# Optimization experiments

Hardware: AMD Instinct MI355X
Metric: run time of the kernel (lower is better)

Reference implementation:

```python
import jax, jax.numpy as jnp
import numpy as np

CUTOFF = 3.0   # self.cutoff
RMIN = 3.5     # rmin in cutoff_function (note rmin > cutoff, faithful to source)
ETA = 4.0
N_RADIAL = 5
N_3BODY = 12
NATOMS = 2048
K = 48         # neighbors per atom (equal counts -> ragged loop becomes dense batch)
HID = 64
NPAIRS = NATOMS * K


def setup_inputs() -> dict:
    key = jax.random.key(0)
    ks = jax.random.split(key, 4)
    # displacements scaled so |rij| is mostly within a few Angstrom
    rij = jax.random.normal(ks[0], (NPAIRS, 3), jnp.float32) * 1.5
    # sorted-by-atom pair list with K neighbors per atom
    unique_i = jnp.repeat(jnp.arange(NATOMS, dtype=jnp.int64), K)
    W1 = jax.random.normal(ks[1], (N_RADIAL + N_3BODY, HID), jnp.float32) * 0.1
    b1 = jnp.zeros((HID,), jnp.float32)
    W2 = jax.random.normal(ks[2], (HID, HID), jnp.float32) * 0.1
    b2 = jnp.zeros((HID,), jnp.float32)
    W3 = jax.random.normal(ks[3], (HID, 1), jnp.float32) * 0.1
    b3 = jnp.zeros((1,), jnp.float32)
    return dict(rij=rij, unique_i=unique_i, W1=W1, b1=b1, W2=W2, b2=b2, W3=W3, b3=b3)


def _energy(rij, W1, b1, W2, b2, W3, b3):
    d = jnp.linalg.norm(rij, axis=1, keepdims=True)           # (P,1)
    diff_norm = rij / jnp.maximum(d, 1e-12)                   # F.normalize
    # pair cutoff (rmin=3.5, c=3.0 as in source)
    fc = jnp.where(d > RMIN,
                   0.5 + 0.5 * jnp.cos(jnp.pi * (d - RMIN) / (CUTOFF - RMIN)),
                   1.0)
    # radial Bessel basis, n = 1..5
    ns = jnp.arange(1, N_RADIAL + 1, dtype=rij.dtype)
    rbf = jnp.sqrt(2.0 / CUTOFF) * jnp.sin(ns * jnp.pi / CUTOFF * d) / d * fc  # (P,5)
    # 3-body Gaussian descriptors
    fcrik = (0.5 + 0.5 * jnp.cos(jnp.pi * d / CUTOFF))[:, 0]  # (P,)
    dn = diff_norm.reshape(NATOMS, K, 3)
    cosang = jnp.einsum('nkd,nld->nkl', dn, dn)               # (N,K,K) pairwise mm
    cosang = jnp.where(jnp.eye(K, dtype=bool)[None], 0.0, cosang)  # fill_diagonal_(0)
    mu = jnp.linspace(-1.0, 1.0, N_3BODY).astype(rij.dtype)
    w = fcrik.reshape(NATOMS, 1, K, 1)                        # fcrik broadcast on axis being summed
    g3b = jnp.sum(jnp.exp(-ETA * (cosang[..., None] - mu) ** 2) * w, axis=2)  # (N,K,12)
    g3b = g3b.reshape(NPAIRS, N_3BODY)
    desc = jnp.concatenate([rbf, g3b], axis=1)                # (P,17)
    h = jnp.tanh(desc @ W1 + b1)
    h = jnp.tanh(h @ W2 + b2)
    eij = h @ W3 + b3                                         # (P,1)
    return jnp.sum(eij * fc)


def reference(rij, unique_i, W1, b1, W2, b2, W3, b3):
    # Module output: gradients of total energy w.r.t. rij (written into beta)
    return jax.grad(_energy)(rij, W1, b1, W2, b2, W3, b3)
```

## Files before the change

### kernel.cpp

```cpp
#include <hip/hip_runtime.h>
#include <hip/hip_bf16.h>

#define NATOMS 2048
#define K 48
#define P (NATOMS * K)
#define NR 5
#define NM 12
#define ND 17
#define HID 64

#define PI_F 3.14159265358979f
#define CUT 3.0f
#define RMIN_F 3.5f
#define AFC (-6.28318530717959f)
#define POC (PI_F / CUT)
#define SQ 0.816496580927726f
#define E1C 1.45454545454545f
#define CMC (-0.132231404958678f)
#define N4L (-5.77078016355585f)
#define E1L (2.09846551402031f)
#define TL2 (2.88539008177793f)

__device__ unsigned short g_w1t[64 * 32];
__device__ unsigned short g_w2t[64 * 64];
__device__ unsigned short g_w2r[64 * 64];
__device__ unsigned short g_w1r[32 * 64];

using frag_ab = __attribute__((ext_vector_type(8))) short;
using frag_cd = __attribute__((ext_vector_type(4))) float;
using f2 = __attribute__((ext_vector_type(2))) float;
using f4 = __attribute__((ext_vector_type(4))) float;

__device__ __forceinline__ float fast_tanh(float x) {
    const float t = __builtin_amdgcn_exp2f(TL2 * x);
    return 1.0f - 2.0f * __builtin_amdgcn_rcpf(t + 1.0f);
}

__device__ __forceinline__ unsigned short f2bs(float x) {
    __hip_bfloat16 b = __float2bfloat16(x);
    return __builtin_bit_cast(unsigned short, b);
}

__global__ __launch_bounds__(256) void k_prep(const float* __restrict__ W1,
                                              const float* __restrict__ W2) {
    const int i = blockIdx.x * 256 + threadIdx.x;
    if (i < 2048) {
        const int n = i >> 5, k = i & 31;
        g_w1t[i] = (k < ND) ? f2bs(W1[k * HID + n]) : (unsigned short)0;
    } else if (i < 2048 + 4096) {
        const int j = i - 2048, n = j >> 6, k = j & 63;
        g_w2t[j] = f2bs(W2[k * HID + n]);
    } else if (i < 2048 + 8192) {
        const int j = i - (2048 + 4096);
        g_w2r[j] = f2bs(W2[j]);
    } else if (i < 2048 + 8192 + 2048) {
        const int j = i - (2048 + 8192), n = j >> 6;
        g_w1r[j] = (n < ND) ? f2bs(W1[j]) : (unsigned short)0;
    }
}

#define SC_OFF    0
#define H1_OFF    9408
#define GZ2_OFF   16320
#define DESC_OFF  23232
#define SGD_OFF   27072
#define SU_OFF    30720
#define SFC_OFF   31488
#define SFK_OFF   31680
#define SCM_OFF   31872
#define SM_BYTES  31920
#define SPART_OFF 9408
#define ST_OFF    16320
#define SGF4_OFF  25728
#define SGU4_OFF  14016
#define SE_OFF    23232

__global__ __launch_bounds__(256, 5) void k_fused(const float* __restrict__ rij,
                                                  const float* __restrict__ b1,
                                                  const float* __restrict__ b2,
                                                  const float* __restrict__ W3,
                                                  const float* __restrict__ b3,
                                                  float* __restrict__ out) {
    __shared__ __align__(16) char smem[SM_BYTES];
    float* sc    = (float*)(smem + SC_OFF);
    short* h1S   = (short*)(smem + H1_OFF);
    short* gz2S  = (short*)(smem + GZ2_OFF);
    short* descS = (short*)(smem + DESC_OFF);
    float* spart = (float*)(smem + SPART_OFF);
    float* sT    = (float*)(smem + ST_OFF);
    float* sgd   = (float*)(smem + SGD_OFF);
    float* su    = (float*)(smem + SU_OFF);
    float* sfc   = (float*)(smem + SFC_OFF);
    float* sfk   = (float*)(smem + SFK_OFF);
    float* scm   = (float*)(smem + SCM_OFF);
    float* se    = (float*)(smem + SE_OFF);
    float* sgf4  = (float*)(smem + SGF4_OFF);
    float* sgu4  = (float*)(smem + SGU4_OFF);

    const int t = threadIdx.x;
    const int base3 = blockIdx.x * (K * 3);

    if (t < K) {
        const float x = rij[base3 + 3 * t];
        const float y = rij[base3 + 3 * t + 1];
        const float z = rij[base3 + 3 * t + 2];
        float s2 = fmaxf(x * x + y * y + z * z, 1e-24f);
        const float inv = __builtin_amdgcn_rsqf(s2);
        const float d = s2 * inv;
        *(f4*)&su[4 * t] = (f4){x * inv, y * inv, z * inv, d};
        sfk[t] = 0.5f + 0.5f * __cosf(POC * d);
        sfc[t] = (d > RMIN_F) ? (0.5f + 0.5f * __cosf(AFC * (d - RMIN_F))) : 1.0f;
#pragma unroll
        for (int c = ND; c < 32; c++) descS[t * 40 + c] = 0;
    }
    if (t >= 64 && t < 64 + NM) {
        const int m = t - 64;
        scm[m] = __expf(CMC * (float)(m * m));
    }
    __syncthreads();

    if (t < 192) {
        const int ch = t / 48, k = t - ch * 48;
        const f4 uk = *(const f4*)&su[4 * k];
        float* scrow = &sc[k * 49 + ch * 12];
        const float* sul = &su[4 * (ch * 12)];
        f2 partv[6];
#pragma unroll
        for (int i = 0; i < 6; i++) partv[i] = (f2){0.0f, 0.0f};
#pragma unroll
        for (int li = 0; li < 12; li++) {
            const int l = ch * 12 + li;
            const f4 ul = *(const f4*)&sul[4 * li];
            float c = uk.x * ul.x + uk.y * ul.y + uk.z * ul.z;
            if (k == l) c = 0.0f;
            scrow[li] = c;
            const float cp1 = c + 1.0f;
            const float e0 = __builtin_amdgcn_exp2f(N4L * cp1 * cp1) * sfk[l];
            const float e1 = __builtin_amdgcn_exp2f(E1L * cp1);
            const float e2s = e1 * e1;
            const f2 e2v = {e2s, e2s};
            f2 tm = {e0, e0 * e1};
            partv[0] += tm;
#pragma unroll
            for (int i = 1; i < 6; i++) { tm *= e2v; partv[i] += tm; }
        }
        float* sp = &spart[(ch * 48 + k) * 13];
#pragma unroll
        for (int i = 0; i < 6; i++) { sp[2 * i] = partv[i].x; sp[2 * i + 1] = partv[i].y; }
    } else {
#pragma unroll
        for (int r = 0; r < 4; r++) {
            const int idx = (t - 192) + 64 * r;
            if (idx < K * NR) {
                const int p = idx / NR, n = idx - NR * p;
                const float d = su[4 * p + 3];
                const float s = SQ * sfc[p] * __builtin_amdgcn_rcpf(d);
                descS[p * 40 + n] = (short)f2bs(s * __sinf((float)(n + 1) * POC * d));
            }
        }
    }
    __syncthreads();

    if (t < 192) {
        const int k = t >> 2, q = t & 3;
#pragma unroll
        for (int i = 0; i < 3; i++) {
            const int m = q * 3 + i;
            const float s = spart[(0 * 48 + k) * 13 + m] + spart[(1 * 48 + k) * 13 + m]
                          + spart[(2 * 48 + k) * 13 + m] + spart[(3 * 48 + k) * 13 + m];
            descS[k * 40 + NR + m] = (short)f2bs(s * scm[m]);
        }
    }
    __syncthreads();

    const int w = t >> 6, lane = t & 63, quad = lane >> 4, lm = lane & 15;
    const int n0 = w * 16 + lm;

    float t1[3][4];
    {
        const frag_ab bf = *(const frag_ab*)&g_w1t[n0 * 32 + quad * 8];
        const float bias = b1[n0];
#pragma unroll
        for (int mt = 0; mt < 3; mt++) {
            const frag_ab a = *(const frag_ab*)&descS[(mt * 16 + lm) * 40 + quad * 8];
            frag_cd acc = {bias, bias, bias, bias};
            acc = __builtin_amdgcn_mfma_f32_16x16x32_bf16(a, bf, acc, 0, 0, 0);
#pragma unroll
            for (int r = 0; r < 4; r++) {
                const float tv = fast_tanh(acc[r]);
                t1[mt][r] = tv;
                h1S[(mt * 16 + quad * 4 + r) * 72 + n0] = (short)f2bs(tv);
            }
        }
    }
    __syncthreads();

    {
        const frag_ab b0 = *(const frag_ab*)&g_w2t[n0 * 64 + quad * 8];
        const frag_ab b1f = *(const frag_ab*)&g_w2t[n0 * 64 + 32 + quad * 8];
        const float bias = b2[n0];
        const float w3n = W3[n0];
#pragma unroll
        for (int mt = 0; mt < 3; mt++) {
            const frag_ab a0 = *(const frag_ab*)&h1S[(mt * 16 + lm) * 72 + quad * 8];
            const frag_ab a1 = *(const frag_ab*)&h1S[(mt * 16 + lm) * 72 + 32 + quad * 8];
            frag_cd acc = {bias, bias, bias, bias};
            acc = __builtin_amdgcn_mfma_f32_16x16x32_bf16(a0, b0, acc, 0, 0, 0);
            acc = __builtin_amdgcn_mfma_f32_16x16x32_bf16(a1, b1f, acc, 0, 0, 0);
            float ep[4];
#pragma unroll
            for (int r = 0; r < 4; r++) {
                const int row = mt * 16 + quad * 4 + r;
                const float tv = fast_tanh(acc[r]);
                ep[r] = tv * w3n;
                gz2S[row * 72 + n0] = (short)f2bs(sfc[row] * w3n * (1.0f - tv * tv));
            }
#pragma unroll
            for (int off = 1; off < 16; off <<= 1) {
#pragma unroll
                for (int r = 0; r < 4; r++) ep[r] += __shfl_xor(ep[r], off, 64);
            }
            if (lm == 0) {
#pragma unroll
                for (int r = 0; r < 4; r++) se[w * 48 + mt * 16 + quad * 4 + r] = ep[r];
            }
        }
    }
    __syncthreads();

    {
        const frag_ab b0 = *(const frag_ab*)&g_w2r[n0 * 64 + quad * 8];
        const frag_ab b1f = *(const frag_ab*)&g_w2r[n0 * 64 + 32 + quad * 8];
#pragma unroll
        for (int mt = 0; mt < 3; mt++) {
            const frag_ab a0 = *(const frag_ab*)&gz2S[(mt * 16 + lm) * 72 + quad * 8];
            const frag_ab a1 = *(const frag_ab*)&gz2S[(mt * 16 + lm) * 72 + 32 + quad * 8];
            frag_cd acc = {0.0f, 0.0f, 0.0f, 0.0f};
            acc = __builtin_amdgcn_mfma_f32_16x16x32_bf16(a0, b0, acc, 0, 0, 0);
            acc = __builtin_amdgcn_mfma_f32_16x16x32_bf16(a1, b1f, acc, 0, 0, 0);
#pragma unroll
            for (int r = 0; r < 4; r++) {
                const float g = acc[r] * (1.0f - t1[mt][r] * t1[mt][r]);
                h1S[(mt * 16 + quad * 4 + r) * 72 + n0] = (short)f2bs(g);
            }
        }
    }
    __syncthreads();

    for (int tid = w; tid < 6; tid += 4) {
        const int mt = tid >> 1, nt = tid & 1, n = nt * 16 + lm;
        const frag_ab b0 = *(const frag_ab*)&g_w1r[n * 64 + quad * 8];
        const frag_ab b1f = *(const frag_ab*)&g_w1r[n * 64 + 32 + quad * 8];
        const frag_ab a0 = *(const frag_ab*)&h1S[(mt * 16 + lm) * 72 + quad * 8];
        const frag_ab a1 = *(const frag_ab*)&h1S[(mt * 16 + lm) * 72 + 32 + quad * 8];
        frag_cd acc = {0.0f, 0.0f, 0.0f, 0.0f};
        acc = __builtin_amdgcn_mfma_f32_16x16x32_bf16(a0, b0, acc, 0, 0, 0);
        acc = __builtin_amdgcn_mfma_f32_16x16x32_bf16(a1, b1f, acc, 0, 0, 0);
        if (n < ND) {
            const float cmul = (n >= NR) ? scm[n - NR] : 1.0f;
#pragma unroll
            for (int r = 0; r < 4; r++)
                sgd[(mt * 16 + quad * 4 + r) * 19 + n] = acc[r] * cmul;
        }
    }
    if (t < K)
        sgd[t * 19 + 17] = se[t] + se[48 + t] + se[96 + t] + se[144 + t] + b3[0];
    __syncthreads();

    if (t < 192) {
        const int ch = t / 48, k = t - ch * 48;
        f2 gm[NM];
#pragma unroll
        for (int m = 0; m < NM; m++) {
            const float g = sgd[k * 19 + NR + m];
            gm[m] = (f2){g, (float)m * g};
        }
        float* scrow = &sc[k * 49 + ch * 12];
        float* strow = &sT[k * 49 + ch * 12];
#pragma unroll
        for (int li = 0; li < 12; li++) {
            const int l = ch * 12 + li;
            const float cp1 = scrow[li] + 1.0f;
            const float e0 = __builtin_amdgcn_exp2f(N4L * cp1 * cp1);
            const float x = __builtin_amdgcn_exp2f(E1L * cp1);
            const f2 xx = {x, x};
            f2 pd = gm[11];
#pragma unroll
            for (int m = 10; m >= 1; m--) pd = __builtin_elementwise_fma(pd, xx, gm[m]);
            const float Pv = fmaf(pd.x, x, gm[0].x);
            const float T = e0 * Pv;
            const float U = e0 * x * pd.y;
            const float Sp = fmaf(cp1, T, -(2.0f / 11.0f) * U);
            strow[li] = T;
            scrow[li] = (k == l) ? 0.0f : (-8.0f) * Sp;
        }
    }
    __syncthreads();

    if (lane < K) {
        float s = 0.0f;
#pragma unroll
        for (int kk = 12 * w; kk < 12 * w + 12; kk++) s += sT[kk * 49 + lane];
        sgf4[w * 48 + lane] = s;

        const int k = lane;
        const float fk = sfk[k];
        float gx = 0.0f, gy = 0.0f, gz = 0.0f;
#pragma unroll
        for (int l = 12 * w; l < 12 * w + 12; l++) {
            const float wgt = fmaf(sc[k * 49 + l], sfk[l], sc[l * 49 + k] * fk);
            const f4 ul = *(const f4*)&su[4 * l];
            gx = fmaf(wgt, ul.x, gx);
            gy = fmaf(wgt, ul.y, gy);
            gz = fmaf(wgt, ul.z, gz);
        }
        sgu4[(w * 48 + k) * 3 + 0] = gx;
        sgu4[(w * 48 + k) * 3 + 1] = gy;
        sgu4[(w * 48 + k) * 3 + 2] = gz;
    }
    __syncthreads();

    if (t < K) {
        const float sgf_t = sgf4[t] + sgf4[48 + t] + sgf4[96 + t] + sgf4[144 + t];
        float gux = 0.0f, guy = 0.0f, guz = 0.0f;
#pragma unroll
        for (int ww = 0; ww < 4; ww++) {
            gux += sgu4[(ww * 48 + t) * 3 + 0];
            guy += sgu4[(ww * 48 + t) * 3 + 1];
            guz += sgu4[(ww * 48 + t) * 3 + 2];
        }
        const f4 uv = *(const f4*)&su[4 * t];
        const float d = uv.w;
        const float ux = uv.x, uy = uv.y, uz = uv.z;
        const float invd = __builtin_amdgcn_rcpf(d);
        float gfc = sgd[t * 19 + 17];
        float gdR = 0.0f;
#pragma unroll
        for (int n = 0; n < NR; n++) {
            const float bn = (float)(n + 1) * POC;
            float sn, cn;
            __sincosf(bn * d, &sn, &cn);
            const float g = sgd[t * 19 + n];
            gfc = fmaf(g, SQ * sn * invd, gfc);
            gdR = fmaf(g, SQ * (bn * cn - sn * invd) * invd, gdR);
        }
        const float fc = sfc[t];
        float dfc = 0.0f;
        if (d > RMIN_F) dfc = -0.5f * AFC * __sinf(AFC * (d - RMIN_F));
        const float dfcrik = -0.5f * POC * __sinf(POC * d);

        const float gd = fc * gdR + gfc * dfc + sgf_t * dfcrik;
        const float dot = gux * ux + guy * uy + guz * uz;

        out[base3 + 3 * t + 0] = fmaf(gd, ux, (gux - dot * ux) * invd);
        out[base3 + 3 * t + 1] = fmaf(gd, uy, (guy - dot * uy) * invd);
        out[base3 + 3 * t + 2] = fmaf(gd, uz, (guz - dot * uz) * invd);
    }
}

extern "C" void kernel_launch(void* const* d_in, const int* in_sizes, int n_in,
                              void* d_out, int out_size, void* d_ws, size_t ws_size,
                              hipStream_t stream) {
    (void)in_sizes; (void)n_in; (void)out_size; (void)d_ws; (void)ws_size;
    const float* rij = (const float*)d_in[0];
    const float* W1 = (const float*)d_in[2];
    const float* b1 = (const float*)d_in[3];
    const float* W2 = (const float*)d_in[4];
    const float* b2 = (const float*)d_in[5];
    const float* W3 = (const float*)d_in[6];
    const float* b3 = (const float*)d_in[7];
    float* out = (float*)d_out;

    k_prep<<<48, 256, 0, stream>>>(W1, W2);
    k_fused<<<NATOMS, 256, 0, stream>>>(rij, b1, b2, W3, b3, out);
}
```

Baseline: 92.75 us.

## Shrink LDS footprint via atomic reductions and cosine recompute to raise occupancy

```diff
diff --git a/kernel.cpp b/kernel.cpp
--- a/kernel.cpp
+++ b/kernel.cpp
@@ -39,6 +39,10 @@
 __device__ __forceinline__ unsigned short f2bs(float x) {
     __hip_bfloat16 b = __float2bfloat16(x);
     return __builtin_bit_cast(unsigned short, b);
+}
+
+__device__ __forceinline__ void lds_add(float* p, float v) {
+    __hip_atomic_fetch_add(p, v, __ATOMIC_RELAXED, __HIP_MEMORY_SCOPE_WORKGROUP);
 }
 
 __global__ __launch_bounds__(256) void k_prep(const float* __restrict__ W1,
@@ -59,47 +63,44 @@
     }
 }
 
-#define SC_OFF    0
-#define H1_OFF    9408
-#define GZ2_OFF   16320
-#define DESC_OFF  23232
-#define SGD_OFF   27072
-#define SU_OFF    30720
-#define SFC_OFF   31488
-#define SFK_OFF   31680
-#define SCM_OFF   31872
-#define SM_BYTES  31920
-#define SPART_OFF 9408
-#define ST_OFF    16320
-#define SGF4_OFF  25728
-#define SGU4_OFF  14016
-#define SE_OFF    23232
-
-__global__ __launch_bounds__(256, 5) void k_fused(const float* __restrict__ rij,
+#define R2_OFF   9408
+#define H1_OFF   13248
+#define SE_OFF   20160
+#define SU_OFF   20928
+#define SFC_OFF  21696
+#define SFK_OFF  21888
+#define SGF_OFF  22080
+#define SGU_OFF  22272
+#define SM_BYTES 23040
+
+__global__ __launch_bounds__(256, 6) void k_fused(const float* __restrict__ rij,
                                                   const float* __restrict__ b1,
                                                   const float* __restrict__ b2,
                                                   const float* __restrict__ W3,
                                                   const float* __restrict__ b3,
                                                   float* __restrict__ out) {
     __shared__ __align__(16) char smem[SM_BYTES];
-    float* sc    = (float*)(smem + SC_OFF);
+    float* g3sum = (float*)(smem);
+    short* gz2S  = (short*)(smem);
+    float* sS    = (float*)(smem);
+    short* descS = (short*)(smem + R2_OFF);
+    float* sgd   = (float*)(smem + R2_OFF);
     short* h1S   = (short*)(smem + H1_OFF);
-    short* gz2S  = (short*)(smem + GZ2_OFF);
-    short* descS = (short*)(smem + DESC_OFF);
-    float* spart = (float*)(smem + SPART_OFF);
-    float* sT    = (float*)(smem + ST_OFF);
-    float* sgd   = (float*)(smem + SGD_OFF);
+    float* se    = (float*)(smem + SE_OFF);
     float* su    = (float*)(smem + SU_OFF);
     float* sfc   = (float*)(smem + SFC_OFF);
     float* sfk   = (float*)(smem + SFK_OFF);
-    float* scm   = (float*)(smem + SCM_OFF);
-    float* se    = (float*)(smem + SE_OFF);
-    float* sgf4  = (float*)(smem + SGF4_OFF);
-    float* sgu4  = (float*)(smem + SGU4_OFF);
+    float* sgf   = (float*)(smem + SGF_OFF);
+    float* sgu   = (float*)(smem + SGU_OFF);
 
     const int t = threadIdx.x;
     const int base3 = blockIdx.x * (K * 3);
 
+    if (t < 156) {
+        *(f4*)(smem + 16 * t) = (f4){0.0f, 0.0f, 0.0f, 0.0f};
+    } else if (t < 216) {
+        *(f4*)(smem + SGF_OFF + 16 * (t - 156)) = (f4){0.0f, 0.0f, 0.0f, 0.0f};
+    }
     if (t < K) {
         const float x = rij[base3 + 3 * t];
         const float y = rij[base3 + 3 * t + 1];
@@ -113,16 +114,11 @@
 #pragma unroll
         for (int c = ND; c < 32; c++) descS[t * 40 + c] = 0;
     }
-    if (t >= 64 && t < 64 + NM) {
-        const int m = t - 64;
-        scm[m] = __expf(CMC * (float)(m * m));
-    }
     __syncthreads();
 
     if (t < 192) {
         const int ch = t / 48, k = t - ch * 48;
         const f4 uk = *(const f4*)&su[4 * k];
-        float* scrow = &sc[k * 49 + ch * 12];
         const float* sul = &su[4 * (ch * 12)];
         f2 partv[6];
 #pragma unroll
@@ -133,7 +129,6 @@
             const f4 ul = *(const f4*)&sul[4 * li];
             float c = uk.x * ul.x + uk.y * ul.y + uk.z * ul.z;
             if (k == l) c = 0.0f;
-            scrow[li] = c;
             const float cp1 = c + 1.0f;
             const float e0 = __builtin_amdgcn_exp2f(N4L * cp1 * cp1) * sfk[l];
             const float e1 = __builtin_amdgcn_exp2f(E1L * cp1);
@@ -144,9 +139,12 @@
 #pragma unroll
             for (int i = 1; i < 6; i++) { tm *= e2v; partv[i] += tm; }
         }
-        float* sp = &spart[(ch * 48 + k) * 13];
-#pragma unroll
-        for (int i = 0; i < 6; i++) { sp[2 * i] = partv[i].x; sp[2 * i + 1] = partv[i].y; }
+        float* gp = &g3sum[k * 13];
+#pragma unroll
+        for (int i = 0; i < 6; i++) {
+            lds_add(&gp[2 * i], partv[i].x);
+            lds_add(&gp[2 * i + 1], partv[i].y);
+        }
     } else {
 #pragma unroll
         for (int r = 0; r < 4; r++) {
@@ -166,9 +164,8 @@
 #pragma unroll
         for (int i = 0; i < 3; i++) {
             const int m = q * 3 + i;
-            const float s = spart[(0 * 48 + k) * 13 + m] + spart[(1 * 48 + k) * 13 + m]
-                          + spart[(2 * 48 + k) * 13 + m] + spart[(3 * 48 + k) * 13 + m];
-            descS[k * 40 + NR + m] = (short)f2bs(s * scm[m]);
+            const float cm = __expf(CMC * (float)(m * m));
+            descS[k * 40 + NR + m] = (short)f2bs(g3sum[k * 13 + m] * cm);
         }
     }
     __syncthreads();
@@ -257,7 +254,8 @@
         acc = __builtin_amdgcn_mfma_f32_16x16x32_bf16(a0, b0, acc, 0, 0, 0);
         acc = __builtin_amdgcn_mfma_f32_16x16x32_bf16(a1, b1f, acc, 0, 0, 0);
         if (n < ND) {
-            const float cmul = (n >= NR) ? scm[n - NR] : 1.0f;
+            const int mm = n - NR;
+            const float cmul = (n >= NR) ? __expf(CMC * (float)(mm * mm)) : 1.0f;
 #pragma unroll
             for (int r = 0; r < 4; r++)
                 sgd[(mt * 16 + quad * 4 + r) * 19 + n] = acc[r] * cmul;
@@ -275,12 +273,17 @@
             const float g = sgd[k * 19 + NR + m];
             gm[m] = (f2){g, (float)m * g};
         }
-        float* scrow = &sc[k * 49 + ch * 12];
-        float* strow = &sT[k * 49 + ch * 12];
+        const f4 uk = *(const f4*)&su[4 * k];
+        int r = k % 12;
+        float gkx = 0.0f, gky = 0.0f, gkz = 0.0f;
 #pragma unroll
         for (int li = 0; li < 12; li++) {
-            const int l = ch * 12 + li;
-            const float cp1 = scrow[li] + 1.0f;
+            const int l = ch * 12 + r;
+            r = (r == 11) ? 0 : r + 1;
+            const f4 ul = *(const f4*)&su[4 * l];
+            float c = uk.x * ul.x + uk.y * ul.y + uk.z * ul.z;
+            if (k == l) c = 0.0f;
+            const float cp1 = c + 1.0f;
             const float e0 = __builtin_amdgcn_exp2f(N4L * cp1 * cp1);
             const float x = __builtin_amdgcn_exp2f(E1L * cp1);
             const f2 xx = {x, x};
@@ -291,44 +294,43 @@
             const float T = e0 * Pv;
             const float U = e0 * x * pd.y;
             const float Sp = fmaf(cp1, T, -(2.0f / 11.0f) * U);
-            strow[li] = T;
-            scrow[li] = (k == l) ? 0.0f : (-8.0f) * Sp;
-        }
+            const float Sv = (k == l) ? 0.0f : (-8.0f) * Sp;
+            sS[k * 49 + l] = Sv;
+            lds_add(&sgf[l], T);
+            const float A = Sv * sfk[l];
+            gkx = fmaf(A, ul.x, gkx);
+            gky = fmaf(A, ul.y, gky);
+            gkz = fmaf(A, ul.z, gkz);
+        }
+        lds_add(&sgu[4 * k + 0], gkx);
+        lds_add(&sgu[4 * k + 1], gky);
+        lds_add(&sgu[4 * k + 2], gkz);
     }
     __syncthreads();
 
     if (lane < K) {
-        float s = 0.0f;
-#pragma unroll
-        for (int kk = 12 * w; kk < 12 * w + 12; kk++) s += sT[kk * 49 + lane];
-        sgf4[w * 48 + lane] = s;
-
         const int k = lane;
+        float t2x = 0.0f, t2y = 0.0f, t2z = 0.0f;
+#pragma unroll
+        for (int l = 12 * w; l < 12 * w + 12; l++) {
+            const float Sv = sS[l * 49 + k];
+            const f4 ul = *(const f4*)&su[4 * l];
+            t2x = fmaf(Sv, ul.x, t2x);
+            t2y = fmaf(Sv, ul.y, t2y);
+            t2z = fmaf(Sv, ul.z, t2z);
+        }
         const float fk = sfk[k];
-        float gx = 0.0f, gy = 0.0f, gz = 0.0f;
-#pragma unroll
-        for (int l = 12 * w; l < 12 * w + 12; l++) {
-            const float wgt = fmaf(sc[k * 49 + l], sfk[l], sc[l * 49 + k] * fk);
-            const f4 ul = *(const f4*)&su[4 * l];
-            gx = fmaf(wgt, ul.x, gx);
-            gy = fmaf(wgt, ul.y, gy);
-            gz = fmaf(wgt, ul.z, gz);
-        }
-        sgu4[(w * 48 + k) * 3 + 0] = gx;
-        sgu4[(w * 48 + k) * 3 + 1] = gy;
-        sgu4[(w * 48 + k) * 3 + 2] = gz;
+        lds_add(&sgu[4 * k + 0], fk * t2x);
+        lds_add(&sgu[4 * k + 1], fk * t2y);
+        lds_add(&sgu[4 * k + 2], fk * t2z);
     }
     __syncthreads();
 
     if (t < K) {
-        const float sgf_t = sgf4[t] + sgf4[48 + t] + sgf4[96 + t] + sgf4[144 + t];
-        float gux = 0.0f, guy = 0.0f, guz = 0.0f;
-#pragma unroll
-        for (int ww = 0; ww < 4; ww++) {
-            gux += sgu4[(ww * 48 + t) * 3 + 0];
-            guy += sgu4[(ww * 48 + t) * 3 + 1];
-            guz += sgu4[(ww * 48 + t) * 3 + 2];
-        }
+        const float sgf_t = sgf[t];
+        const float gux = sgu[4 * t + 0];
+        const float guy = sgu[4 * t + 1];
+        const float guz = sgu[4 * t + 2];
         const f4 uv = *(const f4*)&su[4 * t];
         const float d = uv.w;
         const float ux = uv.x, uy = uv.y, uz = uv.z;
```

Result: slower. 143.6 us (+54.8%).

## Shrink shared memory with bf16 intermediates and shuffle reductions to raise occupancy

Applied to the files above, without the earlier changes.

```diff
diff --git a/kernel.cpp b/kernel.cpp
--- a/kernel.cpp
+++ b/kernel.cpp
@@ -39,6 +39,10 @@
 __device__ __forceinline__ unsigned short f2bs(float x) {
     __hip_bfloat16 b = __float2bfloat16(x);
     return __builtin_bit_cast(unsigned short, b);
+}
+
+__device__ __forceinline__ float bs2f(unsigned short u) {
+    return __builtin_bit_cast(float, ((unsigned)u) << 16);
 }
 
 __global__ __launch_bounds__(256) void k_prep(const float* __restrict__ W1,
@@ -59,43 +63,39 @@
     }
 }
 
-#define SC_OFF    0
-#define H1_OFF    9408
-#define GZ2_OFF   16320
-#define DESC_OFF  23232
-#define SGD_OFF   27072
-#define SU_OFF    30720
-#define SFC_OFF   31488
-#define SFK_OFF   31680
-#define SCM_OFF   31872
-#define SM_BYTES  31920
-#define SPART_OFF 9408
-#define ST_OFF    16320
-#define SGF4_OFF  25728
-#define SGU4_OFF  14016
-#define SE_OFF    23232
-
-__global__ __launch_bounds__(256, 5) void k_fused(const float* __restrict__ rij,
+#define H1_OFF   0
+#define ST_OFF   0
+#define DESC_OFF 6912
+#define GZ2_OFF  6912
+#define SGD_OFF  6912
+#define SGF_OFF  10560
+#define SGU_OFF  11328
+#define SS_OFF   13824
+#define SE_OFF   18528
+#define SU_OFF   19296
+#define SFC_OFF  20064
+#define SFK_OFF  20256
+#define SM_BYTES 20448
+
+__global__ __launch_bounds__(256, 8) void k_fused(const float* __restrict__ rij,
                                                   const float* __restrict__ b1,
                                                   const float* __restrict__ b2,
                                                   const float* __restrict__ W3,
                                                   const float* __restrict__ b3,
                                                   float* __restrict__ out) {
     __shared__ __align__(16) char smem[SM_BYTES];
-    float* sc    = (float*)(smem + SC_OFF);
-    short* h1S   = (short*)(smem + H1_OFF);
-    short* gz2S  = (short*)(smem + GZ2_OFF);
-    short* descS = (short*)(smem + DESC_OFF);
-    float* spart = (float*)(smem + SPART_OFF);
-    float* sT    = (float*)(smem + ST_OFF);
-    float* sgd   = (float*)(smem + SGD_OFF);
-    float* su    = (float*)(smem + SU_OFF);
-    float* sfc   = (float*)(smem + SFC_OFF);
-    float* sfk   = (float*)(smem + SFK_OFF);
-    float* scm   = (float*)(smem + SCM_OFF);
-    float* se    = (float*)(smem + SE_OFF);
-    float* sgf4  = (float*)(smem + SGF4_OFF);
-    float* sgu4  = (float*)(smem + SGU4_OFF);
+    short*          h1S   = (short*)(smem + H1_OFF);
+    unsigned short* sT    = (unsigned short*)(smem + ST_OFF);
+    short*          descS = (short*)(smem + DESC_OFF);
+    short*          gz2S  = (short*)(smem + GZ2_OFF);
+    float*          sgd   = (float*)(smem + SGD_OFF);
+    float*          sgf4  = (float*)(smem + SGF_OFF);
+    float*          sgu4  = (float*)(smem + SGU_OFF);
+    unsigned short* sS    = (unsigned short*)(smem + SS_OFF);
+    float*          se    = (float*)(smem + SE_OFF);
+    float*          su    = (float*)(smem + SU_OFF);
+    float*          sfc   = (float*)(smem + SFC_OFF);
+    float*          sfk   = (float*)(smem + SFK_OFF);
 
     const int t = threadIdx.x;
     const int base3 = blockIdx.x * (K * 3);
@@ -113,16 +113,11 @@
 #pragma unroll
         for (int c = ND; c < 32; c++) descS[t * 40 + c] = 0;
     }
-    if (t >= 64 && t < 64 + NM) {
-        const int m = t - 64;
-        scm[m] = __expf(CMC * (float)(m * m));
-    }
     __syncthreads();
 
     if (t < 192) {
-        const int ch = t / 48, k = t - ch * 48;
+        const int k = t >> 2, ch = t & 3;
         const f4 uk = *(const f4*)&su[4 * k];
-        float* scrow = &sc[k * 49 + ch * 12];
         const float* sul = &su[4 * (ch * 12)];
         f2 partv[6];
 #pragma unroll
@@ -133,7 +128,6 @@
             const f4 ul = *(const f4*)&sul[4 * li];
             float c = uk.x * ul.x + uk.y * ul.y + uk.z * ul.z;
             if (k == l) c = 0.0f;
-            scrow[li] = c;
             const float cp1 = c + 1.0f;
             const float e0 = __builtin_amdgcn_exp2f(N4L * cp1 * cp1) * sfk[l];
             const float e1 = __builtin_amdgcn_exp2f(E1L * cp1);
@@ -144,9 +138,23 @@
 #pragma unroll
             for (int i = 1; i < 6; i++) { tm *= e2v; partv[i] += tm; }
         }
-        float* sp = &spart[(ch * 48 + k) * 13];
-#pragma unroll
-        for (int i = 0; i < 6; i++) { sp[2 * i] = partv[i].x; sp[2 * i + 1] = partv[i].y; }
+#pragma unroll
+        for (int i = 0; i < 6; i++) {
+            partv[i].x += __shfl_xor(partv[i].x, 1);
+            partv[i].y += __shfl_xor(partv[i].y, 1);
+            partv[i].x += __shfl_xor(partv[i].x, 2);
+            partv[i].y += __shfl_xor(partv[i].y, 2);
+        }
+        if (ch == 0) {
+#pragma unroll
+            for (int i = 0; i < 6; i++) {
+                const int m0 = 2 * i, m1 = 2 * i + 1;
+                descS[k * 40 + NR + m0] =
+                    (short)f2bs(partv[i].x * __expf(CMC * (float)(m0 * m0)));
+                descS[k * 40 + NR + m1] =
+                    (short)f2bs(partv[i].y * __expf(CMC * (float)(m1 * m1)));
+            }
+        }
     } else {
 #pragma unroll
         for (int r = 0; r < 4; r++) {
@@ -157,18 +165,6 @@
                 const float s = SQ * sfc[p] * __builtin_amdgcn_rcpf(d);
                 descS[p * 40 + n] = (short)f2bs(s * __sinf((float)(n + 1) * POC * d));
             }
-        }
-    }
-    __syncthreads();
-
-    if (t < 192) {
-        const int k = t >> 2, q = t & 3;
-#pragma unroll
-        for (int i = 0; i < 3; i++) {
-            const int m = q * 3 + i;
-            const float s = spart[(0 * 48 + k) * 13 + m] + spart[(1 * 48 + k) * 13 + m]
-                          + spart[(2 * 48 + k) * 13 + m] + spart[(3 * 48 + k) * 13 + m];
-            descS[k * 40 + NR + m] = (short)f2bs(s * scm[m]);
         }
     }
     __syncthreads();
@@ -257,7 +253,8 @@
         acc = __builtin_amdgcn_mfma_f32_16x16x32_bf16(a0, b0, acc, 0, 0, 0);
         acc = __builtin_amdgcn_mfma_f32_16x16x32_bf16(a1, b1f, acc, 0, 0, 0);
         if (n < ND) {
-            const float cmul = (n >= NR) ? scm[n - NR] : 1.0f;
+            const int mm = n - NR;
+            const float cmul = (n >= NR) ? __expf(CMC * (float)(mm * mm)) : 1.0f;
 #pragma unroll
             for (int r = 0; r < 4; r++)
                 sgd[(mt * 16 + quad * 4 + r) * 19 + n] = acc[r] * cmul;
@@ -268,19 +265,22 @@
     __syncthreads();
 
     if (t < 192) {
-        const int ch = t / 48, k = t - ch * 48;
+        const int k = t >> 2, ch = t & 3;
         f2 gm[NM];
 #pragma unroll
         for (int m = 0; m < NM; m++) {
             const float g = sgd[k * 19 + NR + m];
             gm[m] = (f2){g, (float)m * g};
         }
-        float* scrow = &sc[k * 49 + ch * 12];
-        float* strow = &sT[k * 49 + ch * 12];
+        const f4 uk = *(const f4*)&su[4 * k];
+        const float* sul = &su[4 * (ch * 12)];
 #pragma unroll
         for (int li = 0; li < 12; li++) {
             const int l = ch * 12 + li;
-            const float cp1 = scrow[li] + 1.0f;
+            const f4 ul = *(const f4*)&sul[4 * li];
+            float c = uk.x * ul.x + uk.y * ul.y + uk.z * ul.z;
+            if (k == l) c = 0.0f;
+            const float cp1 = c + 1.0f;
             const float e0 = __builtin_amdgcn_exp2f(N4L * cp1 * cp1);
             const float x = __builtin_amdgcn_exp2f(E1L * cp1);
             const f2 xx = {x, x};
@@ -291,8 +291,9 @@
             const float T = e0 * Pv;
             const float U = e0 * x * pd.y;
             const float Sp = fmaf(cp1, T, -(2.0f / 11.0f) * U);
-            strow[li] = T;
-            scrow[li] = (k == l) ? 0.0f : (-8.0f) * Sp;
+            const float Sv = (k == l) ? 0.0f : (-8.0f) * Sp;
+            sT[k * 49 + l] = f2bs(T);
+            sS[k * 49 + l] = f2bs(Sv);
         }
     }
     __syncthreads();
@@ -300,7 +301,7 @@
     if (lane < K) {
         float s = 0.0f;
 #pragma unroll
-        for (int kk = 12 * w; kk < 12 * w + 12; kk++) s += sT[kk * 49 + lane];
+        for (int kk = 12 * w; kk < 12 * w + 12; kk++) s += bs2f(sT[kk * 49 + lane]);
         sgf4[w * 48 + lane] = s;
 
         const int k = lane;
@@ -308,7 +309,8 @@
         float gx = 0.0f, gy = 0.0f, gz = 0.0f;
 #pragma unroll
         for (int l = 12 * w; l < 12 * w + 12; l++) {
-            const float wgt = fmaf(sc[k * 49 + l], sfk[l], sc[l * 49 + k] * fk);
+            const float wgt = fmaf(bs2f(sS[k * 49 + l]), sfk[l],
+                                   bs2f(sS[l * 49 + k]) * fk);
             const f4 ul = *(const f4*)&su[4 * l];
             gx = fmaf(wgt, ul.x, gx);
             gy = fmaf(wgt, ul.y, gy);
```

After: 92.63 us. About the same (-0.1%).
